# Performance work log

Measured on AMD Instinct MI355X. Metric: run time of the kernel, lower is better.

The kernel has to match this reference:

```python
import jax, jax.numpy as jnp
import numpy as np

N_HEADS = 16


def setup_inputs() -> dict:
    key = jax.random.key(0)
    k1, k2, k3 = jax.random.split(key, 3)
    B, N, D = 2, 2048, 1024
    x = jax.random.normal(k1, (B, N, D), dtype=jnp.float32)
    w_qkv = jax.random.normal(k2, (D, 3 * D), dtype=jnp.float32) * (D ** -0.5)
    w_proj = jax.random.normal(k3, (D, D), dtype=jnp.float32) * (D ** -0.5)
    return {"x": x, "w_qkv": w_qkv, "w_proj": w_proj}


def _rotate_half(t):
    # interleaved-pair rotation: (x1, x2) -> (-x2, x1)
    shp = t.shape
    t2 = t.reshape(*shp[:-1], shp[-1] // 2, 2)
    return jnp.stack((-t2[..., 1], t2[..., 0]), axis=-1).reshape(shp)


def reference(x, w_qkv, w_proj):
    B, N, D = x.shape
    H = N_HEADS
    hd = D // H
    qkv = x @ w_qkv                                   # [B, N, 3D]
    qkv = qkv.reshape(B, N, 3, H, hd).transpose(2, 0, 3, 1, 4)
    q, k, v = qkv[0], qkv[1], qkv[2]                  # [B, H, N, hd]

    inv_freq = 1.0 / (10000.0 ** (jnp.arange(0, hd, 2, dtype=jnp.float32) / hd))
    freqs = jnp.arange(N, dtype=jnp.float32)[:, None] * inv_freq[None, :]  # [N, hd/2]
    sin = jnp.repeat(jnp.sin(freqs), 2, axis=-1)[None, None]               # [1,1,N,hd]
    cos = jnp.repeat(jnp.cos(freqs), 2, axis=-1)[None, None]

    q = q * cos + _rotate_half(q) * sin
    k = k * cos + _rotate_half(k) * sin

    scale = hd ** -0.5
    attn = jax.nn.softmax(jnp.einsum('bhqd,bhkd->bhqk', q, k) * scale, axis=-1)
    out = jnp.einsum('bhqk,bhkd->bhqd', attn, v)      # [B, H, N, hd]
    out = out.transpose(0, 2, 1, 3).reshape(B, N, D)
    return out @ w_proj
```

## Files before the change

### kernel.cpp

```cpp
#include <hip/hip_runtime.h>
#include <hip/hip_bf16.h>
#include <cstdint>
#include <cmath>

#define DEVINL __device__ __forceinline__

typedef __attribute__((ext_vector_type(8)))  __bf16 b8;
typedef __attribute__((ext_vector_type(4)))  float  f4;
typedef __attribute__((ext_vector_type(16))) float  f16v;
typedef __attribute__((ext_vector_type(4)))  unsigned int u32x4;

DEVINL unsigned short f2bf(float f){
  unsigned int u = __float_as_uint(f);
  u += 0x7FFFu + ((u >> 16) & 1u);
  return (unsigned short)(u >> 16);
}

DEVINL void gl_lds16(const void* g, void* l){
  __builtin_amdgcn_global_load_lds(
      (const __attribute__((address_space(1))) void*)g,
      (__attribute__((address_space(3))) void*)l, 16, 0, 0);
}

DEVINL f4 mfma16(b8 a, b8 b, f4 c){
  return __builtin_amdgcn_mfma_f32_16x16x32_bf16(a, b, c, 0, 0, 0);
}
DEVINL f16v mfma32(b8 a, b8 b, f16v c){
  return __builtin_amdgcn_mfma_f32_32x32x16_bf16(a, b, c, 0, 0, 0);
}

DEVINL float exp2a(float x){
  float r; asm("v_exp_f32 %0, %1" : "=v"(r) : "v"(x)); return r;
}
DEVINL unsigned int cvtpk(float lo, float hi){
  unsigned int r; asm("v_cvt_pk_bf16_f32 %0, %1, %2" : "=v"(r) : "v"(lo), "v"(hi)); return r;
}
DEVINL void plswap(unsigned int &a, unsigned int &b){
  asm("v_permlane32_swap_b32 %0, %1" : "+v"(a), "+v"(b));
}

#define BARRAW() asm volatile("s_barrier" ::: "memory")
#define WCNT(N)  asm volatile("s_waitcnt vmcnt(" #N ")" ::: "memory")


__global__ __launch_bounds__(256) void cast_bf16_k(const float* __restrict__ in,
                                                   unsigned short* __restrict__ out, int n4){
  int stride = gridDim.x * blockDim.x;
  for (int i = blockIdx.x * blockDim.x + threadIdx.x; i < n4; i += stride){
    float4 v = ((const float4*)in)[i];
    ushort4 o; o.x = f2bf(v.x); o.y = f2bf(v.y); o.z = f2bf(v.z); o.w = f2bf(v.w);
    ((ushort4*)out)[i] = o;
  }
}

__global__ __launch_bounds__(256) void transpose_cast_k(const float* __restrict__ in,
                                                        unsigned short* __restrict__ out,
                                                        int K, int N){
  __shared__ float t[32][33];
  int nx = blockIdx.x * 32, kx = blockIdx.y * 32;
  int tx = threadIdx.x & 31, ty = threadIdx.x >> 5;
  #pragma unroll
  for (int i = 0; i < 4; i++)
    t[ty + 8*i][tx] = in[(size_t)(kx + ty + 8*i) * N + nx + tx];
  __syncthreads();
  #pragma unroll
  for (int i = 0; i < 4; i++)
    out[(size_t)(nx + ty + 8*i) * K + kx + tx] = f2bf(t[tx][ty + 8*i]);
}

__global__ __launch_bounds__(256) void rope_tab_k(float2* __restrict__ rt){
  int t = blockIdx.x * 256 + threadIdx.x;
  int n = t >> 5, i = t & 31;
  float invf = expf(-(float)i * (9.210340371976184f / 32.0f));
  float ph = (float)n * invf;
  float s, c;
  sincosf(ph, &s, &c);
  rt[t] = make_float2(c, s);
}


template<int NREP, int EPI>
__global__ __launch_bounds__(512, 2) void gemm256_k(const unsigned short* __restrict__ A,
                                                    const unsigned short* __restrict__ Bt, int N,
                                                    float* __restrict__ Of,
                                                    unsigned short* __restrict__ Qg,
                                                    unsigned short* __restrict__ Kg,
                                                    unsigned short* __restrict__ Vt,
                                                    const float2* __restrict__ rtab){
  constexpr int K = 1024;
  __shared__ unsigned short As[2][256 * 64];
  __shared__ unsigned short Bs[2][NREP * 64 * 64];
  const int tid = threadIdx.x, w = tid >> 6, l = tid & 63;
  const int wm = w >> 2, wn = w & 3;
  const int m0 = blockIdx.y * 256, n0 = blockIdx.x * (NREP * 64);

  f4 acc[8][NREP];
  const f4 fz = {0.f, 0.f, 0.f, 0.f};
  #pragma unroll
  for (int i = 0; i < 8; i++)
    #pragma unroll
    for (int j = 0; j < NREP; j++) acc[i][j] = fz;

  const int srow8 = (l >> 3);
  const int ssrc  = ((l & 7) ^ (srow8 & 7)) * 8;

  auto stage = [&](int slot, int kt){
    const unsigned short* Ab = A + kt * 64 + ssrc;
    #pragma unroll
    for (int c2 = 0; c2 < 4; c2++){
      int ch = w * 4 + c2;
      gl_lds16(Ab + (size_t)(m0 + ch * 8 + srow8) * K, (char*)&As[slot][0] + ch * 1024);
    }
    const unsigned short* Bb = Bt + kt * 64 + ssrc;
    #pragma unroll
    for (int c2 = 0; c2 < NREP; c2++){
      int ch = w * NREP + c2;
      gl_lds16(Bb + (size_t)(n0 + ch * 8 + srow8) * K, (char*)&Bs[slot][0] + ch * 1024);
    }
  };

  auto compute = [&](int slot){
    const char* At  = (const char*)&As[slot][0];
    const char* Btl = (const char*)&Bs[slot][0];
    #pragma unroll
    for (int kk = 0; kk < 2; kk++){
      b8 af[8], bf[NREP];
      int sb = kk * 4 + (l >> 4);
      #pragma unroll
      for (int mi = 0; mi < 8; mi++){
        int r = wm * 128 + mi * 16 + (l & 15);
        af[mi] = *(const b8*)(At + r * 128 + ((sb ^ (r & 7)) * 16));
      }
      #pragma unroll
      for (int ni = 0; ni < NREP; ni++){
        int r = wn * (NREP * 16) + ni * 16 + (l & 15);
        bf[ni] = *(const b8*)(Btl + r * 128 + ((sb ^ (r & 7)) * 16));
      }
      __builtin_amdgcn_s_setprio(1);
      #pragma unroll
      for (int mi = 0; mi < 8; mi++)
        #pragma unroll
        for (int ni = 0; ni < NREP; ni++)
          acc[mi][ni] = mfma16(af[mi], bf[ni], acc[mi][ni]);
      __builtin_amdgcn_s_setprio(0);
    }
  };

  auto wcnt_stg = [&](){
    if constexpr (NREP == 4)      WCNT(8);
    else if constexpr (NREP == 3) WCNT(7);
    else if constexpr (NREP == 2) WCNT(6);
    else                          WCNT(5);
  };

  stage(0, 0);
  stage(1, 1);
  wcnt_stg();
  BARRAW();
  for (int i = 0; i < 8; i++){
    compute(0);
    BARRAW();
    if (i < 7){ stage(0, 2 * i + 2); wcnt_stg(); }
    else      { WCNT(0); }
    BARRAW();
    compute(1);
    BARRAW();
    if (i < 7){ stage(1, 2 * i + 3); wcnt_stg(); }
    BARRAW();
  }

  if constexpr (EPI == 0){
    const float qscale = 0.18033688011112042f;
    const int bb2 = m0 >> 11;
    #pragma unroll
    for (int mi = 0; mi < 8; mi++){
      #pragma unroll
      for (int ni = 0; ni < NREP; ni++){
        f4 a = acc[mi][ni];
        int c = n0 + wn * (NREP * 16) + ni * 16 + (l & 15);
        int s = c >> 10;
        int d = c & 63, h = (c >> 6) & 15;
        if (s == 2){
          int ns0 = (m0 & 2047) + wm * 128 + mi * 16 + (l >> 4) * 4;
          ushort4 pv;
          pv.x = f2bf(a[0]); pv.y = f2bf(a[1]); pv.z = f2bf(a[2]); pv.w = f2bf(a[3]);
          *(ushort4*)(Vt + (((size_t)(bb2 * 16 + h) * 64 + d) << 11) + ns0) = pv;
        } else {
          #pragma unroll
          for (int jj = 0; jj < 4; jj++){
            int m = m0 + wm * 128 + mi * 16 + (l >> 4) * 4 + jj;
            int bb = m >> 11, ns = m & 2047;
            size_t didx = ((size_t)(bb * 16 + h) * 2048 + ns) * 64 + d;
            float part = __shfl_xor(a[jj], 1);
            float2 cs = rtab[ns * 32 + (d >> 1)];
            float val = (d & 1) ? (a[jj] * cs.x + part * cs.y)
                                : (a[jj] * cs.x - part * cs.y);
            if (s == 0){ Qg[didx] = f2bf(val * qscale); }
            else       { Kg[didx] = f2bf(val); }
          }
        }
      }
    }
  } else {
    #pragma unroll
    for (int mi = 0; mi < 8; mi++)
      #pragma unroll
      for (int ni = 0; ni < NREP; ni++){
        int c = n0 + wn * (NREP * 16) + ni * 16 + (l & 15);
        #pragma unroll
        for (int jj = 0; jj < 4; jj++){
          int m = m0 + wm * 128 + mi * 16 + (l >> 4) * 4 + jj;
          Of[(size_t)m * N + c] = acc[mi][ni][jj];
        }
      }
  }
}


__global__ __launch_bounds__(256) void attn_k(const unsigned short* __restrict__ Qg,
                                              const unsigned short* __restrict__ Kg,
                                              const unsigned short* __restrict__ Vt,
                                              unsigned short* __restrict__ Ao){
  __shared__ unsigned short Ks[2][4096];
  __shared__ unsigned short Vs[2][4096];
  const int tid = threadIdx.x, w = tid >> 6, l = tid & 63;
  const int l31 = l & 31, lam = l >> 5;

  const int id = blockIdx.x + blockIdx.y * 16;
  const int xc = id & 7, j = id >> 3;
  const int g = xc * 4 + (j & 3), qb = j >> 2;
  const int q0 = qb * 128 + w * 32;
  const size_t hb = (size_t)g << 17;

  b8 qf[4];
  {
    const unsigned short* qrow = Qg + hb + (size_t)(q0 + l31) * 64 + lam * 8;
    #pragma unroll
    for (int kd = 0; kd < 4; kd++) qf[kd] = *(const b8*)(qrow + kd * 16);
  }

  const unsigned short* kgb = Kg + hb;
  const unsigned short* vgb = Vt + hb;
  const int srow = (l >> 3);
  const int sc8  = ((l & 7) ^ (srow & 7)) * 8;

  auto stage = [&](int buf, int kv0){
    #pragma unroll
    for (int c = 0; c < 2; c++){
      int chunk = w * 2 + c;
      int r = chunk * 8 + srow;
      gl_lds16(kgb + (size_t)(kv0 + r) * 64 + sc8,
               (char*)&Ks[buf][0] + chunk * 1024);
      gl_lds16(vgb + (size_t)r * 2048 + kv0 + sc8,
               (char*)&Vs[buf][0] + chunk * 1024);
    }
  };

  union { u32x4 u; b8 v; } ones;
  ones.u[0] = ones.u[1] = ones.u[2] = ones.u[3] = 0x3F803F80u;

  f16v O[2], L;
  #pragma unroll
  for (int i = 0; i < 16; i++){ O[0][i] = 0.f; O[1][i] = 0.f; L[i] = 0.f; }

  auto tile = [&](int buf){
    b8 kf[8], vf[8];
    const char* ksb = (const char*)&Ks[buf][0];
    const char* vsb = (const char*)&Vs[buf][0];
    const int rsw = (l31 & 7);
    #pragma unroll
    for (int kvb = 0; kvb < 2; kvb++)
      #pragma unroll
      for (int kd = 0; kd < 4; kd++)
        kf[kvb * 4 + kd] = *(const b8*)(ksb + (kvb * 32 + l31) * 128
                                        + (((kd * 2 + lam) ^ rsw) * 16));
    #pragma unroll
    for (int s = 0; s < 4; s++)
      #pragma unroll
      for (int db = 0; db < 2; db++)
        vf[s * 2 + db] = *(const b8*)(vsb + (db * 32 + l31) * 128
                                      + (((2 * s + lam) ^ rsw) * 16));

    f16v st[2];
    #pragma unroll
    for (int i = 0; i < 16; i++){ st[0][i] = 0.f; st[1][i] = 0.f; }
    #pragma unroll
    for (int kd = 0; kd < 4; kd++) st[0] = mfma32(kf[kd],     qf[kd], st[0]);
    #pragma unroll
    for (int kd = 0; kd < 4; kd++) st[1] = mfma32(kf[4 + kd], qf[kd], st[1]);

    #pragma unroll
    for (int b2 = 0; b2 < 2; b2++)
      #pragma unroll
      for (int r = 0; r < 16; r++)
        st[b2][r] = exp2a(st[b2][r]);

    #pragma unroll
    for (int s = 0; s < 4; s++){
      const int b = s >> 1, base = (s & 1) * 8;
      unsigned int pA = cvtpk(st[b][base + 0], st[b][base + 1]);
      unsigned int pB = cvtpk(st[b][base + 2], st[b][base + 3]);
      unsigned int pC = cvtpk(st[b][base + 4], st[b][base + 5]);
      unsigned int pD = cvtpk(st[b][base + 6], st[b][base + 7]);
      plswap(pA, pC); plswap(pB, pD);
      union { u32x4 u; b8 v; } pf;
      pf.u[0] = pA; pf.u[1] = pB; pf.u[2] = pC; pf.u[3] = pD;
      O[0] = mfma32(pf.v, vf[s * 2 + 0], O[0]);
      O[1] = mfma32(pf.v, vf[s * 2 + 1], O[1]);
      L    = mfma32(pf.v, ones.v,       L);
    }
  };

  stage(0, 0);
  stage(1, 64);
  WCNT(4);
  BARRAW();
  for (int i = 0; i < 16; i++){
    tile(0);
    BARRAW();
    if (i < 15){ stage(0, (2 * i + 2) * 64); WCNT(4); }
    else       { WCNT(0); }
    BARRAW();
    tile(1);
    BARRAW();
    if (i < 15){ stage(1, (2 * i + 3) * 64); WCNT(4); }
    BARRAW();
  }

  const int bb = g >> 4, h = g & 15;
  unsigned short* aoBase = Ao + (size_t)bb * 2048 * 1024 + h * 64 + l31;
  #pragma unroll
  for (int r = 0; r < 16; r++){
    int qr = (r & 3) + 8 * (r >> 2) + 4 * lam;
    float li = 1.0f / L[r];
    size_t rowoff = (size_t)(q0 + qr) * 1024;
    aoBase[rowoff]      = f2bf(O[0][r] * li);
    aoBase[rowoff + 32] = f2bf(O[1][r] * li);
  }
}


extern "C" void kernel_launch(void* const* d_in, const int* in_sizes, int n_in,
                              void* d_out, int out_size, void* d_ws, size_t ws_size,
                              hipStream_t stream){
  const float* x     = (const float*)d_in[0];
  const float* wqkv  = (const float*)d_in[1];
  const float* wproj = (const float*)d_in[2];
  float* out = (float*)d_out;

  if (ws_size < 42467328u) return;
  char* ws = (char*)d_ws;
  unsigned short* xb     = (unsigned short*)(ws);
  unsigned short* wqkvT  = (unsigned short*)(ws + 8388608);
  unsigned short* wprojT = (unsigned short*)(ws + 14680064);
  float2*         rtab   = (float2*)(ws + 16777216);
  unsigned short* Qg     = (unsigned short*)(ws + 17301504);
  unsigned short* Kg     = (unsigned short*)(ws + 25690112);
  unsigned short* Vt     = (unsigned short*)(ws + 34078720);
  unsigned short* Ao     = xb;

  cast_bf16_k<<<2048, 256, 0, stream>>>(x, xb, 4096 * 1024 / 4);
  transpose_cast_k<<<dim3(96, 32), 256, 0, stream>>>(wqkv, wqkvT, 1024, 3072);
  transpose_cast_k<<<dim3(32, 32), 256, 0, stream>>>(wproj, wprojT, 1024, 1024);
  rope_tab_k<<<256, 256, 0, stream>>>(rtab);
  gemm256_k<3, 0><<<dim3(16, 16), 512, 0, stream>>>(xb, wqkvT, 3072, nullptr, Qg, Kg, Vt, rtab);
  attn_k<<<dim3(16, 32), 256, 0, stream>>>(Qg, Kg, Vt, Ao);
  gemm256_k<1, 1><<<dim3(16, 16), 512, 0, stream>>>(Ao, wprojT, 1024, out, nullptr, nullptr, nullptr, nullptr);
}
```

Measured before the change: 116.1 us.

## Give each attention wave 64 query rows and compute row sums on VALU

The attention kernel now assigns two 32-row query blocks to each wave, so each staged K/V tile in LDS serves 64 query rows instead of 32, and the grid is halved. The softmax denominator is no longer built with an extra MFMA against a ones vector. It is now accumulated as per-lane scalar sums of the exponentials, combined across half-waves with a shuffle, and broadcast to output rows with another shuffle. This cuts LDS reads and matrix-core work per query. In exchange it doubles accumulator register use and leaves only 256 blocks of 4 waves, about one block per CU, which reduces latency hiding.

Result: slower. 124.8 us (+7.5%).

```diff
diff --git a/kernel.cpp b/kernel.cpp
--- a/kernel.cpp
+++ b/kernel.cpp
@@ -217,10 +217,10 @@
 }
 
 
-__global__ __launch_bounds__(256) void attn_k(const unsigned short* __restrict__ Qg,
-                                              const unsigned short* __restrict__ Kg,
-                                              const unsigned short* __restrict__ Vt,
-                                              unsigned short* __restrict__ Ao){
+__global__ __launch_bounds__(256, 1) void attn_k(const unsigned short* __restrict__ Qg,
+                                                 const unsigned short* __restrict__ Kg,
+                                                 const unsigned short* __restrict__ Vt,
+                                                 unsigned short* __restrict__ Ao){
   __shared__ unsigned short Ks[2][4096];
   __shared__ unsigned short Vs[2][4096];
   const int tid = threadIdx.x, w = tid >> 6, l = tid & 63;
@@ -228,15 +228,16 @@
 
   const int id = blockIdx.x + blockIdx.y * 16;
   const int xc = id & 7, j = id >> 3;
-  const int g = xc * 4 + (j & 3), qb = j >> 2;
-  const int q0 = qb * 128 + w * 32;
+  const int g = xc * 4 + (j & 3), qseg = j >> 2;
+  const int q0 = qseg * 256 + w * 64;
   const size_t hb = (size_t)g << 17;
 
-  b8 qf[4];
-  {
-    const unsigned short* qrow = Qg + hb + (size_t)(q0 + l31) * 64 + lam * 8;
-    #pragma unroll
-    for (int kd = 0; kd < 4; kd++) qf[kd] = *(const b8*)(qrow + kd * 16);
+  b8 qf[2][4];
+  #pragma unroll
+  for (int qb = 0; qb < 2; qb++){
+    const unsigned short* qrow = Qg + hb + (size_t)(q0 + qb * 32 + l31) * 64 + lam * 8;
+    #pragma unroll
+    for (int kd = 0; kd < 4; kd++) qf[qb][kd] = *(const b8*)(qrow + kd * 16);
   }
 
   const unsigned short* kgb = Kg + hb;
@@ -256,58 +257,60 @@
     }
   };
 
-  union { u32x4 u; b8 v; } ones;
-  ones.u[0] = ones.u[1] = ones.u[2] = ones.u[3] = 0x3F803F80u;
-
-  f16v O[2], L;
-  #pragma unroll
-  for (int i = 0; i < 16; i++){ O[0][i] = 0.f; O[1][i] = 0.f; L[i] = 0.f; }
+  f16v O[2][2];
+  float lrow[2] = {0.f, 0.f};
+  #pragma unroll
+  for (int a = 0; a < 2; a++)
+    #pragma unroll
+    for (int b = 0; b < 2; b++)
+      #pragma unroll
+      for (int i = 0; i < 16; i++) O[a][b][i] = 0.f;
 
   auto tile = [&](int buf){
-    b8 kf[8], vf[8];
     const char* ksb = (const char*)&Ks[buf][0];
     const char* vsb = (const char*)&Vs[buf][0];
     const int rsw = (l31 & 7);
     #pragma unroll
-    for (int kvb = 0; kvb < 2; kvb++)
+    for (int kvh = 0; kvh < 2; kvh++){
+      b8 kf[4];
       #pragma unroll
       for (int kd = 0; kd < 4; kd++)
-        kf[kvb * 4 + kd] = *(const b8*)(ksb + (kvb * 32 + l31) * 128
-                                        + (((kd * 2 + lam) ^ rsw) * 16));
-    #pragma unroll
-    for (int s = 0; s < 4; s++)
-      #pragma unroll
-      for (int db = 0; db < 2; db++)
-        vf[s * 2 + db] = *(const b8*)(vsb + (db * 32 + l31) * 128
-                                      + (((2 * s + lam) ^ rsw) * 16));
-
-    f16v st[2];
-    #pragma unroll
-    for (int i = 0; i < 16; i++){ st[0][i] = 0.f; st[1][i] = 0.f; }
-    #pragma unroll
-    for (int kd = 0; kd < 4; kd++) st[0] = mfma32(kf[kd],     qf[kd], st[0]);
-    #pragma unroll
-    for (int kd = 0; kd < 4; kd++) st[1] = mfma32(kf[4 + kd], qf[kd], st[1]);
-
-    #pragma unroll
-    for (int b2 = 0; b2 < 2; b2++)
-      #pragma unroll
-      for (int r = 0; r < 16; r++)
-        st[b2][r] = exp2a(st[b2][r]);
-
-    #pragma unroll
-    for (int s = 0; s < 4; s++){
-      const int b = s >> 1, base = (s & 1) * 8;
-      unsigned int pA = cvtpk(st[b][base + 0], st[b][base + 1]);
-      unsigned int pB = cvtpk(st[b][base + 2], st[b][base + 3]);
-      unsigned int pC = cvtpk(st[b][base + 4], st[b][base + 5]);
-      unsigned int pD = cvtpk(st[b][base + 6], st[b][base + 7]);
-      plswap(pA, pC); plswap(pB, pD);
-      union { u32x4 u; b8 v; } pf;
-      pf.u[0] = pA; pf.u[1] = pB; pf.u[2] = pC; pf.u[3] = pD;
-      O[0] = mfma32(pf.v, vf[s * 2 + 0], O[0]);
-      O[1] = mfma32(pf.v, vf[s * 2 + 1], O[1]);
-      L    = mfma32(pf.v, ones.v,       L);
+        kf[kd] = *(const b8*)(ksb + (kvh * 32 + l31) * 128
+                              + (((kd * 2 + lam) ^ rsw) * 16));
+      b8 vf[2][2];
+      #pragma unroll
+      for (int s2 = 0; s2 < 2; s2++)
+        #pragma unroll
+        for (int db = 0; db < 2; db++)
+          vf[s2][db] = *(const b8*)(vsb + (db * 32 + l31) * 128
+                                    + (((4 * kvh + 2 * s2 + lam) ^ rsw) * 16));
+      #pragma unroll
+      for (int qb = 0; qb < 2; qb++){
+        f16v st;
+        #pragma unroll
+        for (int i = 0; i < 16; i++) st[i] = 0.f;
+        #pragma unroll
+        for (int kd = 0; kd < 4; kd++) st = mfma32(kf[kd], qf[qb][kd], st);
+        float ps = 0.f;
+        #pragma unroll
+        for (int r = 0; r < 16; r++){
+          float p = exp2a(st[r]); st[r] = p; ps += p;
+        }
+        lrow[qb] += ps;
+        #pragma unroll
+        for (int s2 = 0; s2 < 2; s2++){
+          const int base = s2 * 8;
+          unsigned int pA = cvtpk(st[base + 0], st[base + 1]);
+          unsigned int pB = cvtpk(st[base + 2], st[base + 3]);
+          unsigned int pC = cvtpk(st[base + 4], st[base + 5]);
+          unsigned int pD = cvtpk(st[base + 6], st[base + 7]);
+          plswap(pA, pC); plswap(pB, pD);
+          union { u32x4 u; b8 v; } pf;
+          pf.u[0] = pA; pf.u[1] = pB; pf.u[2] = pC; pf.u[3] = pD;
+          O[qb][0] = mfma32(pf.v, vf[s2][0], O[qb][0]);
+          O[qb][1] = mfma32(pf.v, vf[s2][1], O[qb][1]);
+        }
+      }
     }
   };
 
@@ -330,12 +333,17 @@
   const int bb = g >> 4, h = g & 15;
   unsigned short* aoBase = Ao + (size_t)bb * 2048 * 1024 + h * 64 + l31;
   #pragma unroll
-  for (int r = 0; r < 16; r++){
-    int qr = (r & 3) + 8 * (r >> 2) + 4 * lam;
-    float li = 1.0f / L[r];
-    size_t rowoff = (size_t)(q0 + qr) * 1024;
-    aoBase[rowoff]      = f2bf(O[0][r] * li);
-    aoBase[rowoff + 32] = f2bf(O[1][r] * li);
+  for (int qb = 0; qb < 2; qb++){
+    float lr = lrow[qb] + __shfl_xor(lrow[qb], 32);
+    float linv = 1.0f / lr;
+    #pragma unroll
+    for (int r = 0; r < 16; r++){
+      int qr = (r & 3) + 8 * (r >> 2) + 4 * lam;
+      float li = __shfl(linv, qr);
+      size_t rowoff = (size_t)(q0 + qb * 32 + qr) * 1024;
+      aoBase[rowoff]      = f2bf(O[qb][0][r] * li);
+      aoBase[rowoff + 32] = f2bf(O[qb][1][r] * li);
+    }
   }
 }
 
@@ -364,6 +372,6 @@
   transpose_cast_k<<<dim3(32, 32), 256, 0, stream>>>(wproj, wprojT, 1024, 1024);
   rope_tab_k<<<256, 256, 0, stream>>>(rtab);
   gemm256_k<3, 0><<<dim3(16, 16), 512, 0, stream>>>(xb, wqkvT, 3072, nullptr, Qg, Kg, Vt, rtab);
-  attn_k<<<dim3(16, 32), 256, 0, stream>>>(Qg, Kg, Vt, Ao);
+  attn_k<<<dim3(16, 16), 256, 0, stream>>>(Qg, Kg, Vt, Ao);
   gemm256_k<1, 1><<<dim3(16, 16), 512, 0, stream>>>(Ao, wprojT, 1024, out, nullptr, nullptr, nullptr, nullptr);
 }
```
